# Kernel tuning notes

Hardware: AMD Instinct MI355X
Metric: run time of the kernel (lower is better)

Reference implementation:

```python
import jax, jax.numpy as jnp
import numpy as np

EMBED_DIM = 1024
NUM_HEADS = 16
HEAD_DIM = EMBED_DIM // NUM_HEADS


def setup_inputs() -> dict:
    key = jax.random.key(0)
    ks = jax.random.split(key, 9)
    bs, seq_len = 4, 2048
    s = 1.0 / np.sqrt(EMBED_DIM)
    return {
        "x": jax.random.normal(ks[0], (bs, seq_len, EMBED_DIM), jnp.float32),
        "wq": jax.random.uniform(ks[1], (EMBED_DIM, EMBED_DIM), jnp.float32, -s, s),
        "bq": jax.random.uniform(ks[2], (EMBED_DIM,), jnp.float32, -s, s),
        "wk": jax.random.uniform(ks[3], (EMBED_DIM, EMBED_DIM), jnp.float32, -s, s),
        "bk": jax.random.uniform(ks[4], (EMBED_DIM,), jnp.float32, -s, s),
        "wv": jax.random.uniform(ks[5], (EMBED_DIM, EMBED_DIM), jnp.float32, -s, s),
        "bv": jax.random.uniform(ks[6], (EMBED_DIM,), jnp.float32, -s, s),
        "wo": jax.random.uniform(ks[7], (EMBED_DIM, EMBED_DIM), jnp.float32, -s, s),
        "bo": jax.random.uniform(ks[8], (EMBED_DIM,), jnp.float32, -s, s),
    }


def reference(x, wq, bq, wk, bk, wv, bv, wo, bo):
    bs, seq_len, _ = x.shape
    # projections (torch Linear: y = x @ W.T + b; here w stored as [out,in])
    q = x @ wq.T + bq
    k = x @ wk.T + bk
    v = x @ wv.T + bv
    # split heads -> (bs, heads, seq, head_dim)
    def split(t):
        return t.reshape(bs, seq_len, NUM_HEADS, HEAD_DIM).transpose(0, 2, 1, 3)
    q, k, v = split(q), split(k), split(v)
    scale = 1.0 / jnp.sqrt(jnp.asarray(HEAD_DIM, jnp.float32))
    scores = jnp.einsum("bhqd,bhkd->bhqk", q, k) * scale
    attn = jax.nn.softmax(scores, axis=-1)
    out = jnp.einsum("bhqk,bhkd->bhqd", attn, v)
    out = out.transpose(0, 2, 1, 3).reshape(bs, seq_len, EMBED_DIM)
    return out @ wo.T + bo
```

## Files before the change

kernel.cpp:

```cpp
#include <hip/hip_runtime.h>
#include <stdint.h>

#define SEQ 2048
#define BSZ 4
#define NH 16
#define HD 64
#define EMB 1024
#define NT (SEQ / 64)
#define QSCALE 0.1803368801111f

using bf16x8 = __attribute__((ext_vector_type(8))) __bf16;
using u16x8  = __attribute__((ext_vector_type(8))) unsigned short;
using u32x4  = __attribute__((ext_vector_type(4))) uint32_t;
using f32x4  = __attribute__((ext_vector_type(4))) float;
using f32x16 = __attribute__((ext_vector_type(16))) float;

__device__ __forceinline__ float exp2v(float x) { return __builtin_amdgcn_exp2f(x); }

__device__ __forceinline__ unsigned short f2bf(float f) {
    union { float f; uint32_t u; } v; v.f = f;
    uint32_t r = v.u + 0x7fffu + ((v.u >> 16) & 1u);
    return (unsigned short)(r >> 16);
}

__device__ __forceinline__ uint32_t cvtpk(float lo, float hi) {
    uint32_t r;
    asm("v_cvt_pk_bf16_f32 %0, %1, %2" : "=v"(r) : "v"(lo), "v"(hi));
    return r;
}
__device__ __forceinline__ void plswap(uint32_t& a, uint32_t& b) {
    asm volatile("v_permlane32_swap_b32 %0, %1" : "+v"(a), "+v"(b));
}

__device__ __forceinline__ void gload16(void* lds, const void* g) {
    __builtin_amdgcn_global_load_lds(
        (const __attribute__((address_space(1))) void*)g,
        (__attribute__((address_space(3))) void*)lds, 16, 0, 0);
}

__global__ void cast_kernel(const float* __restrict__ s, unsigned short* __restrict__ d, int n) {
    int i = (blockIdx.x * blockDim.x + threadIdx.x) * 4;
    if (i + 3 >= n) {
        for (int j = 0; j < 4 && i + j < n; ++j) d[i + j] = f2bf(s[i + j]);
        return;
    }
    float4 v = *(const float4*)(s + i);
    ushort4 o;
    o.x = f2bf(v.x); o.y = f2bf(v.y); o.z = f2bf(v.z); o.w = f2bf(v.w);
    *(ushort4*)(d + i) = o;
}

template <int MODE>
__global__ __launch_bounds__(256, 2)
void gemm_bt(const unsigned short* __restrict__ A,
             const unsigned short* __restrict__ Bw,
             const float* __restrict__ b0, const float* __restrict__ b1,
             const float* __restrict__ b2,
             void* __restrict__ C0, void* __restrict__ C1, void* __restrict__ C2,
             int M, int N, int Kd) {
    __shared__ unsigned short As[128][64];
    __shared__ unsigned short Bs[128][64];

    const int t    = threadIdx.x;
    const int lane = t & 63;
    const int wid  = t >> 6;
    const int g    = lane >> 4;
    const int lr   = lane & 15;
    const int wm   = wid >> 1, wn = wid & 1;
    const int m0   = blockIdx.x * 128, n0 = blockIdx.y * 128;
    const int srow = lane >> 3;
    const int scol = (lane & 7) * 8;

    f32x4 acc[4][4];
    const f32x4 zero = {0.f, 0.f, 0.f, 0.f};
#pragma unroll
    for (int i = 0; i < 4; ++i)
#pragma unroll
        for (int j = 0; j < 4; ++j) acc[i][j] = zero;

    for (int kt = 0; kt < Kd; kt += 64) {
#pragma unroll
        for (int p = 0; p < 4; ++p) {
            int rowA = wid * 32 + p * 8;
            gload16(&As[rowA][0], A  + (size_t)(m0 + rowA + srow) * Kd + kt + scol);
            gload16(&Bs[rowA][0], Bw + (size_t)(n0 + rowA + srow) * Kd + kt + scol);
        }
        __syncthreads();
#pragma unroll
        for (int ks = 0; ks < 2; ++ks) {
            bf16x8 af[4], bfr[4];
#pragma unroll
            for (int m = 0; m < 4; ++m)
                af[m] = *(const bf16x8*)&As[wm * 64 + m * 16 + lr][ks * 32 + g * 8];
#pragma unroll
            for (int n = 0; n < 4; ++n)
                bfr[n] = *(const bf16x8*)&Bs[wn * 64 + n * 16 + lr][ks * 32 + g * 8];
#pragma unroll
            for (int m = 0; m < 4; ++m)
#pragma unroll
                for (int n = 0; n < 4; ++n)
                    acc[m][n] = __builtin_amdgcn_mfma_f32_16x16x32_bf16(af[m], bfr[n], acc[m][n], 0, 0, 0);
        }
        __syncthreads();
    }

    int seg = MODE == 2 ? (n0 >> 10) : 0;
    if (MODE == 2 && seg == 2) {
        unsigned short* CwT = (unsigned short*)C2;
        int nl = n0 & 1023;
#pragma unroll
        for (int n = 0; n < 4; ++n) {
            int colL = nl + wn * 64 + n * 16 + lr;
            float bv = b2[colL];
#pragma unroll
            for (int m = 0; m < 4; ++m) {
                int rowg = m0 + wm * 64 + m * 16 + g * 4;
                int bb = rowg >> 11, seq = rowg & 2047;
                ushort4 w;
                w.x = f2bf(acc[m][n][0] + bv);
                w.y = f2bf(acc[m][n][1] + bv);
                w.z = f2bf(acc[m][n][2] + bv);
                w.w = f2bf(acc[m][n][3] + bv);
                *(ushort4*)(CwT + ((size_t)(bb * 1024 + colL)) * SEQ + seq) = w;
            }
        }
        return;
    }

    const float* bias;
    unsigned short* Cw = nullptr;
    float* Cf = nullptr;
    float scl = 1.0f;
    int nl;
    if (MODE == 2) {
        bias = seg == 0 ? b0 : b1;
        Cw = (unsigned short*)(seg == 0 ? C0 : C1);
        scl = seg == 0 ? QSCALE : 1.0f;
        nl = n0 & 1023;
    } else {
        bias = b0; Cf = (float*)C0; nl = n0;
    }
#pragma unroll
    for (int n = 0; n < 4; ++n) {
        int colL = nl + wn * 64 + n * 16 + lr;
        float bv = bias[colL];
#pragma unroll
        for (int m = 0; m < 4; ++m) {
            int rowg = m0 + wm * 64 + m * 16 + g * 4;
#pragma unroll
            for (int r = 0; r < 4; ++r) {
                float val = (acc[m][n][r] + bv) * scl;
                if (MODE == 2)
                    Cw[(size_t)(rowg + r) * EMB + colL] = f2bf(val);
                else
                    Cf[(size_t)(rowg + r) * EMB + colL] = val;
            }
        }
    }
}

__global__ __launch_bounds__(512, 4)
void flash_attn(const unsigned short* __restrict__ Q,
                const unsigned short* __restrict__ K,
                const unsigned short* __restrict__ VT,
                unsigned short* __restrict__ O) {
    __shared__ unsigned char KsB[2][64 * 128];
    __shared__ unsigned char VtB[2][64 * 128];

    const int nwg  = gridDim.x * gridDim.y * gridDim.z;
    const int cpx  = nwg >> 3;
    const int bid0 = (blockIdx.z * gridDim.y + blockIdx.y) * gridDim.x + blockIdx.x;
    const int bid  = (bid0 % 8) * cpx + (bid0 / 8);
    const int bx   = bid & (gridDim.x - 1);
    const int h    = (bid >> 3) & 15;
    const int b    = bid >> 7;

    const int t    = threadIdx.x;
    const int wid  = t >> 6;
    const int lane = t & 63;
    const int l31  = lane & 31;
    const int hi   = lane >> 5;
    const int hi16 = hi << 4;
    const int sw   = (l31 & 7) << 4;
    const int qbase = bx * 256 + wid * 32;
    const size_t rowbase = (size_t)b * SEQ;
    const unsigned short* Kh  = K + rowbase * EMB + h * HD;
    const unsigned short* Vth = VT + (size_t)(b * 1024 + h * HD) * SEQ;

    const int grow = t >> 3;
    const int gc16 = (t & 7) ^ (grow & 7);
    const unsigned short* Ksrc0 = Kh  + (size_t)grow * EMB + gc16 * 8;
    const unsigned short* Vsrc0 = Vth + (size_t)grow * SEQ + gc16 * 8;

    bf16x8 qf[4];
#pragma unroll
    for (int db = 0; db < 4; ++db)
        qf[db] = *(const bf16x8*)(Q + (rowbase + qbase + l31) * EMB + h * HD + db * 16 + hi * 8);

    bf16x8 vones;
#pragma unroll
    for (int j = 0; j < 8; ++j) vones[j] = (__bf16)1.0f;

    f32x16 o0, o1, o2;
#pragma unroll
    for (int r = 0; r < 16; ++r) { o0[r] = 0.f; o1[r] = 0.f; o2[r] = 0.f; }
    float me = -1e30f;

    auto issue_tile = [&](int kt) {
        unsigned char* Ks = KsB[kt & 1] + wid * 1024;
        unsigned char* Vt = VtB[kt & 1] + wid * 1024;
        gload16(Ks, Ksrc0 + (size_t)kt * 64 * EMB);
        gload16(Vt, Vsrc0 + kt * 64);
    };
    issue_tile(0);

    for (int kt = 0; kt < NT; ++kt) {
        unsigned char* Ks = KsB[kt & 1];
        unsigned char* Vt = VtB[kt & 1];

        __syncthreads();

        if (kt + 1 < NT) issue_tile(kt + 1);

        f32x16 s0, s1;
#pragma unroll
        for (int r = 0; r < 16; ++r) { s0[r] = 0.f; s1[r] = 0.f; }
        __builtin_amdgcn_s_setprio(1);
#pragma unroll
        for (int db = 0; db < 4; ++db) {
            bf16x8 kf0 = *(const bf16x8*)(Ks + l31 * 128        + ((db * 32 + hi16) ^ sw));
            bf16x8 kf1 = *(const bf16x8*)(Ks + (l31 + 32) * 128 + ((db * 32 + hi16) ^ sw));
            s0 = __builtin_amdgcn_mfma_f32_32x32x16_bf16(kf0, qf[db], s0, 0, 0, 0);
            s1 = __builtin_amdgcn_mfma_f32_32x32x16_bf16(kf1, qf[db], s1, 0, 0, 0);
        }
        __builtin_amdgcn_s_setprio(0);

        float pm = fmaxf(fmaxf(s0[0], s0[1]), s0[2]);
#pragma unroll
        for (int r = 3; r < 15; r += 2) pm = fmaxf(fmaxf(pm, s0[r]), s0[r + 1]);
        pm = fmaxf(pm, s0[15]);
#pragma unroll
        for (int r = 0; r < 16; r += 2) pm = fmaxf(fmaxf(pm, s1[r]), s1[r + 1]);
        pm = fmaxf(pm, __shfl_xor(pm, 32));

        if (!__all(pm - me <= 8.0f)) {
            float mn = fmaxf(me, pm);
            float al = exp2v(me - mn);
            me = mn;
#pragma unroll
            for (int r = 0; r < 16; ++r) {
                int addr = hi16 + (((r & 3) + 8 * (r >> 2)) << 2);
                float ar = __int_as_float(
                    __builtin_amdgcn_ds_bpermute(addr, __float_as_int(al)));
                o0[r] *= ar; o1[r] *= ar; o2[r] *= ar;
            }
        }

        s0 = s0 - me;
        s1 = s1 - me;
#pragma unroll
        for (int r = 0; r < 16; ++r) s0[r] = exp2v(s0[r]);
#pragma unroll
        for (int r = 0; r < 16; ++r) s1[r] = exp2v(s1[r]);

        bf16x8 pa[4];
#pragma unroll
        for (int kb = 0; kb < 2; ++kb) {
            uint32_t dw[8];
#pragma unroll
            for (int i = 0; i < 8; ++i)
                dw[i] = kb == 0 ? cvtpk(s0[2 * i], s0[2 * i + 1])
                                : cvtpk(s1[2 * i], s1[2 * i + 1]);
            plswap(dw[0], dw[2]); plswap(dw[1], dw[3]);
            plswap(dw[4], dw[6]); plswap(dw[5], dw[7]);
            u32x4 w0 = {dw[0], dw[1], dw[2], dw[3]};
            u32x4 w1 = {dw[4], dw[5], dw[6], dw[7]};
            pa[kb * 2]     = __builtin_bit_cast(bf16x8, w0);
            pa[kb * 2 + 1] = __builtin_bit_cast(bf16x8, w1);
        }

        __builtin_amdgcn_s_setprio(1);
#pragma unroll
        for (int kk = 0; kk < 4; ++kk) {
            bf16x8 vf0 = *(const bf16x8*)(Vt + l31 * 128        + ((kk * 32 + hi16) ^ sw));
            bf16x8 vf1 = *(const bf16x8*)(Vt + (l31 + 32) * 128 + ((kk * 32 + hi16) ^ sw));
            o0 = __builtin_amdgcn_mfma_f32_32x32x16_bf16(pa[kk], vf0, o0, 0, 0, 0);
            o1 = __builtin_amdgcn_mfma_f32_32x32x16_bf16(pa[kk], vf1, o1, 0, 0, 0);
            o2 = __builtin_amdgcn_mfma_f32_32x32x16_bf16(pa[kk], vones, o2, 0, 0, 0);
        }
        __builtin_amdgcn_s_setprio(0);
    }

#pragma unroll
    for (int r = 0; r < 16; ++r) {
        float inv = 1.0f / o2[r];
        int q = qbase + (r & 3) + 8 * (r >> 2) + 4 * hi;
        size_t ro = (rowbase + q) * EMB + h * HD;
        O[ro + l31]      = f2bf(o0[r] * inv);
        O[ro + 32 + l31] = f2bf(o1[r] * inv);
    }
}

extern "C" void kernel_launch(void* const* d_in, const int* in_sizes, int n_in,
                              void* d_out, int out_size, void* d_ws, size_t ws_size,
                              hipStream_t stream) {
    const float* x  = (const float*)d_in[0];
    const float* wq = (const float*)d_in[1];
    const float* bq = (const float*)d_in[2];
    const float* wk = (const float*)d_in[3];
    const float* bk = (const float*)d_in[4];
    const float* wv = (const float*)d_in[5];
    const float* bv = (const float*)d_in[6];
    const float* wo = (const float*)d_in[7];
    const float* bo = (const float*)d_in[8];

    char* ws = (char*)d_ws;
    const size_t M = (size_t)BSZ * SEQ;
    unsigned short* xb    = (unsigned short*)ws;
    unsigned short* wqkvb = (unsigned short*)(ws + (size_t)16 * 1024 * 1024);
    unsigned short* wob   = (unsigned short*)(ws + (size_t)22 * 1024 * 1024);
    unsigned short* Qb    = (unsigned short*)(ws + (size_t)24 * 1024 * 1024);
    unsigned short* Kb    = Qb + M * EMB;
    unsigned short* VTb   = Kb + M * EMB;

    const int nX = (int)(M * EMB);
    cast_kernel<<<nX / 1024, 256, 0, stream>>>(x, xb, nX);
    cast_kernel<<<1024, 256, 0, stream>>>(wq, wqkvb,                 EMB * EMB);
    cast_kernel<<<1024, 256, 0, stream>>>(wk, wqkvb + 1024 * 1024,   EMB * EMB);
    cast_kernel<<<1024, 256, 0, stream>>>(wv, wqkvb + 2 * 1024 * 1024, EMB * EMB);
    cast_kernel<<<1024, 256, 0, stream>>>(wo, wob, EMB * EMB);

    gemm_bt<2><<<dim3(64, 24), 256, 0, stream>>>(xb, wqkvb, bq, bk, bv,
                                                 Qb, Kb, VTb, (int)M, 3 * EMB, EMB);

    flash_attn<<<dim3(SEQ / 256, NH, BSZ), 512, 0, stream>>>(Qb, Kb, VTb, xb);

    gemm_bt<0><<<dim3(64, 8), 256, 0, stream>>>(xb, wob, bo, nullptr, nullptr,
                                                d_out, nullptr, nullptr, (int)M, EMB, EMB);
}
```

Baseline: 204.6 us.

## Double-buffer GEMM LDS tiles, swizzle workgroup order, fuse weight casts

The GEMM now stages the next K-tile into a second LDS buffer while computing on the current one, which removes the load-then-wait stall at each iteration. It also remaps workgroup IDs so that groups of eight consecutive IDs are spread across the grid, which is meant to improve cache locality across XCDs. The four weight cast launches are merged into one launch that picks its source and destination from blockIdx.y. LDS use doubles, to 64KB per block, which may reduce occupancy. The tile remap hardcodes 64 M-tiles, which matches both GEMM launches.

Result: slower. 220.7 us (+7.9%).

```diff
diff --git a/kernel.cpp b/kernel.cpp
--- a/kernel.cpp
+++ b/kernel.cpp
@@ -44,6 +44,24 @@
         for (int j = 0; j < 4 && i + j < n; ++j) d[i + j] = f2bf(s[i + j]);
         return;
     }
+    float4 v = *(const float4*)(s + i);
+    ushort4 o;
+    o.x = f2bf(v.x); o.y = f2bf(v.y); o.z = f2bf(v.z); o.w = f2bf(v.w);
+    *(ushort4*)(d + i) = o;
+}
+
+__global__ void cast4_kernel(const float* __restrict__ w0, const float* __restrict__ w1,
+                             const float* __restrict__ w2, const float* __restrict__ w3,
+                             unsigned short* __restrict__ d0, unsigned short* __restrict__ d1,
+                             unsigned short* __restrict__ d2, unsigned short* __restrict__ d3) {
+    const float* s; unsigned short* d;
+    switch (blockIdx.y) {
+        case 0:  s = w0; d = d0; break;
+        case 1:  s = w1; d = d1; break;
+        case 2:  s = w2; d = d2; break;
+        default: s = w3; d = d3; break;
+    }
+    int i = (blockIdx.x * blockDim.x + threadIdx.x) * 4;
     float4 v = *(const float4*)(s + i);
     ushort4 o;
     o.x = f2bf(v.x); o.y = f2bf(v.y); o.z = f2bf(v.z); o.w = f2bf(v.w);
@@ -58,8 +76,8 @@
              const float* __restrict__ b2,
              void* __restrict__ C0, void* __restrict__ C1, void* __restrict__ C2,
              int M, int N, int Kd) {
-    __shared__ unsigned short As[128][64];
-    __shared__ unsigned short Bs[128][64];
+    __shared__ unsigned short As[2][128][64];
+    __shared__ unsigned short Bs[2][128][64];
 
     const int t    = threadIdx.x;
     const int lane = t & 63;
@@ -67,7 +85,14 @@
     const int g    = lane >> 4;
     const int lr   = lane & 15;
     const int wm   = wid >> 1, wn = wid & 1;
-    const int m0   = blockIdx.x * 128, n0 = blockIdx.y * 128;
+
+    const int nwg  = gridDim.x * gridDim.y;
+    const int cpx  = nwg >> 3;
+    const int orig = blockIdx.y * gridDim.x + blockIdx.x;
+    const int f    = (orig & 7) * cpx + (orig >> 3);
+    const int m0   = (f & 63) * 128;
+    const int n0   = (f >> 6) * 128;
+
     const int srow = lane >> 3;
     const int scol = (lane & 7) * 8;
 
@@ -78,23 +103,30 @@
 #pragma unroll
         for (int j = 0; j < 4; ++j) acc[i][j] = zero;
 
-    for (int kt = 0; kt < Kd; kt += 64) {
+    auto stage = [&](int buf, int kt) {
 #pragma unroll
         for (int p = 0; p < 4; ++p) {
             int rowA = wid * 32 + p * 8;
-            gload16(&As[rowA][0], A  + (size_t)(m0 + rowA + srow) * Kd + kt + scol);
-            gload16(&Bs[rowA][0], Bw + (size_t)(n0 + rowA + srow) * Kd + kt + scol);
-        }
-        __syncthreads();
+            gload16(&As[buf][rowA][0], A  + (size_t)(m0 + rowA + srow) * Kd + kt + scol);
+            gload16(&Bs[buf][rowA][0], Bw + (size_t)(n0 + rowA + srow) * Kd + kt + scol);
+        }
+    };
+
+    const int nkt = Kd >> 6;
+    stage(0, 0);
+    __syncthreads();
+    int buf = 0;
+    for (int kt = 0; kt < nkt; ++kt) {
+        if (kt + 1 < nkt) stage(buf ^ 1, (kt + 1) << 6);
 #pragma unroll
         for (int ks = 0; ks < 2; ++ks) {
             bf16x8 af[4], bfr[4];
 #pragma unroll
             for (int m = 0; m < 4; ++m)
-                af[m] = *(const bf16x8*)&As[wm * 64 + m * 16 + lr][ks * 32 + g * 8];
+                af[m] = *(const bf16x8*)&As[buf][wm * 64 + m * 16 + lr][ks * 32 + g * 8];
 #pragma unroll
             for (int n = 0; n < 4; ++n)
-                bfr[n] = *(const bf16x8*)&Bs[wn * 64 + n * 16 + lr][ks * 32 + g * 8];
+                bfr[n] = *(const bf16x8*)&Bs[buf][wn * 64 + n * 16 + lr][ks * 32 + g * 8];
 #pragma unroll
             for (int m = 0; m < 4; ++m)
 #pragma unroll
@@ -102,6 +134,7 @@
                     acc[m][n] = __builtin_amdgcn_mfma_f32_16x16x32_bf16(af[m], bfr[n], acc[m][n], 0, 0, 0);
         }
         __syncthreads();
+        buf ^= 1;
     }
 
     int seg = MODE == 2 ? (n0 >> 10) : 0;
@@ -325,10 +358,9 @@
 
     const int nX = (int)(M * EMB);
     cast_kernel<<<nX / 1024, 256, 0, stream>>>(x, xb, nX);
-    cast_kernel<<<1024, 256, 0, stream>>>(wq, wqkvb,                 EMB * EMB);
-    cast_kernel<<<1024, 256, 0, stream>>>(wk, wqkvb + 1024 * 1024,   EMB * EMB);
-    cast_kernel<<<1024, 256, 0, stream>>>(wv, wqkvb + 2 * 1024 * 1024, EMB * EMB);
-    cast_kernel<<<1024, 256, 0, stream>>>(wo, wob, EMB * EMB);
+    cast4_kernel<<<dim3(1024, 4), 256, 0, stream>>>(
+        wq, wk, wv, wo,
+        wqkvb, wqkvb + 1024 * 1024, wqkvb + 2 * 1024 * 1024, wob);
 
     gemm_bt<2><<<dim3(64, 24), 256, 0, stream>>>(xb, wqkvb, bq, bk, bv,
                                                  Qb, Kb, VTb, (int)M, 3 * EMB, EMB);
```
